# Kernel optimization log

Measured on AMD Instinct MI355X. Metric: run time of the kernel, lower is better.

## Reference

```python
import jax, jax.numpy as jnp
import numpy as np
from jax import lax

B = 1024      # batch
L = 529       # token sequence length (becomes conv channels after permute)
E = 100       # embedding size (becomes conv steps after permute)
V = 15245     # vocab size
F = 16        # conv filters
U = 100       # LSTM units
ALPHA = 0.2   # leaky_relu negative slope (keras.ops.leaky_relu default)


def setup_inputs() -> dict:
    key = jax.random.key(0)
    ks = jax.random.split(key, 8)
    tokens = jax.random.randint(ks[0], (B, L), 0, V)
    # Embedding: keras 'uniform' initializer (-0.05, 0.05)
    emb = jax.random.uniform(ks[1], (V, E), minval=-0.05, maxval=0.05, dtype=jnp.float32)
    # Conv1D kernel [width, in_ch, out_ch], HeNormal
    conv_w = jax.random.normal(ks[2], (2, L, F), dtype=jnp.float32) * np.sqrt(2.0 / (2 * L))
    conv_b = jnp.zeros((F,), jnp.float32)
    # LSTM kernels: [in, 4U] and [U, 4U], gate order i,f,g,o; unit_forget_bias=1
    k_lstm = jax.random.normal(ks[3], (F, 4 * U), dtype=jnp.float32) * np.sqrt(1.0 / F)
    rk_lstm = jax.random.normal(ks[4], (U, 4 * U), dtype=jnp.float32) * np.sqrt(1.0 / U)
    b_lstm = jnp.concatenate([jnp.zeros((U,)), jnp.ones((U,)), jnp.zeros((2 * U,))]).astype(jnp.float32)
    w1 = jax.random.normal(ks[5], (U, 64), dtype=jnp.float32) * np.sqrt(1.0 / U)
    b1 = jnp.zeros((64,), jnp.float32)
    w2 = jax.random.normal(ks[6], (64, 3), dtype=jnp.float32) * np.sqrt(1.0 / 64)
    b2 = jnp.zeros((3,), jnp.float32)
    return dict(tokens=tokens, emb=emb, conv_w=conv_w, conv_b=conv_b,
                k_lstm=k_lstm, rk_lstm=rk_lstm, b_lstm=b_lstm,
                w1=w1, b1=b1, w2=w2, b2=b2)


def _leaky(v):
    return jnp.where(v >= 0, v, ALPHA * v)


def reference(tokens, emb, conv_w, conv_b, k_lstm, rk_lstm, b_lstm, w1, b1, w2, b2):
    x = emb[tokens]                       # [B, 529, 100]
    x = jnp.transpose(x, (0, 2, 1))       # [B, 100, 529]  (steps=100, channels=529)
    x = lax.conv_general_dilated(x, conv_w, window_strides=(2,), padding='SAME',
                                 dimension_numbers=('NWC', 'WIO', 'NWC'))
    x = jax.nn.relu(x + conv_b)           # [B, 50, 16]
    b, lo, c = x.shape
    x = x.reshape(b, lo // 2, 2, c).max(axis=2)  # max_pool k=2 s=2 -> [B, 25, 16]

    # LSTM with activation=leaky_relu, recurrent_activation=sigmoid, gates i,f,g,o
    zx = jnp.einsum('btc,cu->btu', x, k_lstm) + b_lstm  # precompute input proj [B, 25, 4U]

    def step(carry, z_t):
        h, cst = carry
        z = z_t + h @ rk_lstm
        i, f, g, o = jnp.split(z, 4, axis=-1)
        i = jax.nn.sigmoid(i)
        f = jax.nn.sigmoid(f)
        o = jax.nn.sigmoid(o)
        cst = f * cst + i * _leaky(g)
        h = o * _leaky(cst)
        return (h, cst), None

    h0 = jnp.zeros((b, U), x.dtype)
    (h, _), _ = lax.scan(step, (h0, h0), jnp.swapaxes(zx, 0, 1))  # scan over 25 steps

    d = jnp.tanh(h @ w1 + b1)             # dropout is identity at inference
    return jax.nn.softmax(d @ w2 + b2, axis=-1)  # [B, 3]
```

## Files before the change

### kernel.cpp

```cpp
#include <hip/hip_runtime.h>
#include <hip/hip_bf16.h>

#define B_  1024
#define LA  529
#define EE  100
#define NF  16
#define NT  50
#define NS  25
#define NU  100
#define NJ  400
#define NKC 34

typedef float        f32x4v __attribute__((ext_vector_type(4)));
typedef short        s16x8  __attribute__((ext_vector_type(8)));
typedef unsigned int u32x4  __attribute__((ext_vector_type(4)));
typedef _Float16     h2v    __attribute__((ext_vector_type(2)));
typedef _Float16     h16x8  __attribute__((ext_vector_type(8)));

__device__ __forceinline__ float leaky(float v) { return v >= 0.f ? v : 0.2f * v; }

__device__ __forceinline__ unsigned int pkh2(float x, float y) {
    auto p = __builtin_amdgcn_cvt_pkrtz(x, y);
    return __builtin_bit_cast(unsigned int, p);
}
__device__ __forceinline__ unsigned short f2h(float x) {
    return __builtin_bit_cast(unsigned short, (_Float16)x);
}

__global__ __launch_bounds__(256) void prep_kernel(
    const float* __restrict__ emb,
    const float* __restrict__ conv_w,
    const float* __restrict__ k_lstm,
    const float* __restrict__ rk,
    const float* __restrict__ b_lstm,
    unsigned int*   __restrict__ emb_h,
    unsigned int*   __restrict__ convw_h,
    unsigned short* __restrict__ wfl)
{
    const int gid = blockIdx.x * 256 + threadIdx.x;
    const int stride = gridDim.x * 256;
    for (int i = gid; i < (15245 * 100) / 2; i += stride) {
        const float2 v = ((const float2*)emb)[i];
        emb_h[i] = pkh2(v.x, v.y);
    }
    for (int i = gid; i < LA * NF; i += stride)
        convw_h[i] = pkh2(conv_w[i], conv_w[LA * NF + i]);
    for (int n = gid; n < 25 * 2048; n += stride) {
        const int tile = n >> 11, c = (n >> 9) & 3, l = (n >> 3) & 63, e = n & 7;
        const int jg = tile * 16 + (l & 15);
        const int k  = c * 32 + ((l >> 4) << 3) + e;
        float x = 0.f;
        if (k < NU)        x = rk[k * NJ + jg];
        else if (k < 116)  x = k_lstm[(k - NU) * NJ + jg];
        else if (k == 116) x = b_lstm[jg];
        wfl[n] = f2h(x);
    }
}

__global__ __launch_bounds__(256, 2) void conv_mfma_kernel(
    const int*          __restrict__ tokens,
    const unsigned int* __restrict__ emb_h,
    const unsigned int* __restrict__ convw_h,
    const float*        __restrict__ conv_b,
    float*              __restrict__ p_out)
{
    __shared__ __align__(16) unsigned int wf[NKC * 64 * 4];
    __shared__ int tok2[2 * LA];

    const int tid  = threadIdx.x;
    const int lane = tid & 63;
    const int wid  = tid >> 6;
    const int bb   = wid >> 1;
    const int tp   = wid & 1;
    const int b    = blockIdx.x * 2 + bb;

    if (tid < 256) {
        const int j = tid & 3, l = (tid >> 2) & 63;
        if (!(((l >> 4) == 0) && (j == 0)))
            wf[(NKC - 1) * 256 + tid] = 0u;
    }
    for (int i = tid; i < LA * NF; i += 256) {
        const int c = i >> 4, f = i & 15;
        wf[(((c >> 4) * 64 + ((c >> 2) & 3) * 16 + f) << 2) + (c & 3)] = convw_h[i];
    }
    for (int i = tid; i < 2 * LA; i += 256)
        tok2[i] = tokens[(size_t)blockIdx.x * 2 * LA + i];
    __syncthreads();

    const int r = lane & 15;
    const int q = lane >> 4;
    const int m0 = tp * 2, m1 = m0 + 1;
    int tr0 = m0 * 16 + r; tr0 = tr0 > 49 ? 49 : tr0;
    int tr1 = m1 * 16 + r; tr1 = tr1 > 49 ? 49 : tr1;
    const int* __restrict__ tk = tok2 + bb * LA;

    f32x4v ac0 = {0.f, 0.f, 0.f, 0.f}, ac1 = {0.f, 0.f, 0.f, 0.f};

#define LOAD_A(s_, A0, A1) do { \
    const int s2 = (s_); \
    _Pragma("unroll") \
    for (int j = 0; j < 4; ++j) { \
        int c = 16 * s2 + 4 * q + j; \
        if (c >= LA) c = 0; \
        const size_t rowb = (size_t)tk[c] * 50; \
        (A0)[j] = emb_h[rowb + tr0]; \
        (A1)[j] = emb_h[rowb + tr1]; \
    } } while (0)

    u32x4 Aa0, Aa1, Ab0, Ab1, An0, An1;
    LOAD_A(0, Aa0, Aa1);
    LOAD_A(1, Ab0, Ab1);
#pragma unroll
    for (int s = 0; s < NKC; ++s) {
        if (s + 2 < NKC) LOAD_A(s + 2, An0, An1);
        const u32x4 Bv = ((const u32x4*)wf)[s * 64 + lane];
        ac0 = __builtin_amdgcn_mfma_f32_16x16x32_f16(
            __builtin_bit_cast(h16x8, Aa0), __builtin_bit_cast(h16x8, Bv), ac0, 0, 0, 0);
        ac1 = __builtin_amdgcn_mfma_f32_16x16x32_f16(
            __builtin_bit_cast(h16x8, Aa1), __builtin_bit_cast(h16x8, Bv), ac1, 0, 0, 0);
        Aa0 = Ab0; Aa1 = Ab1; Ab0 = An0; Ab1 = An1;
    }
#undef LOAD_A

    const float bf = conv_b[r];
    {
        const float y0 = fmaxf(ac0[0] + bf, 0.f), y1 = fmaxf(ac0[1] + bf, 0.f);
        const float y2 = fmaxf(ac0[2] + bf, 0.f), y3 = fmaxf(ac0[3] + bf, 0.f);
        const int s0 = m0 * 8 + 2 * q;
        if (s0 < NS)     p_out[(size_t)b * (NS * NF) + s0 * NF + r]       = fmaxf(y0, y1);
        if (s0 + 1 < NS) p_out[(size_t)b * (NS * NF) + (s0 + 1) * NF + r] = fmaxf(y2, y3);
    }
    {
        const float y0 = fmaxf(ac1[0] + bf, 0.f), y1 = fmaxf(ac1[1] + bf, 0.f);
        const float y2 = fmaxf(ac1[2] + bf, 0.f), y3 = fmaxf(ac1[3] + bf, 0.f);
        const int s0 = m1 * 8 + 2 * q;
        if (s0 < NS)     p_out[(size_t)b * (NS * NF) + s0 * NF + r]       = fmaxf(y0, y1);
        if (s0 + 1 < NS) p_out[(size_t)b * (NS * NF) + (s0 + 1) * NF + r] = fmaxf(y2, y3);
    }
}

__global__ __launch_bounds__(896) void lstm_mfma_kernel(
    const float* __restrict__ p_in,
    const unsigned short* __restrict__ wfl,
    const float* __restrict__ w1,
    const float* __restrict__ b1,
    const float* __restrict__ w2,
    const float* __restrict__ b2,
    float*       __restrict__ out)
{
    __shared__ __align__(16) unsigned short a_lds[2][4][64][8];
    __shared__ __align__(16) float z_lds[NJ][4];
    __shared__ float h_f32[4][NU];
    __shared__ float d_lds[4 * 64];

    const int tid  = threadIdx.x;
    const int lane = tid & 63;
    const int wid  = tid >> 6;
    const int b0   = blockIdx.x * 4;

    for (int i = tid; i < 2 * 4 * 64 * 8; i += 896) ((unsigned short*)a_lds)[i] = 0;

    const int t0 = (wid * 2     < 25) ? wid * 2     : 0;
    const int t1 = (wid * 2 + 1 < 25) ? wid * 2 + 1 : 0;
    h16x8 bfr[2][4];
#pragma unroll
    for (int c = 0; c < 4; ++c) {
        bfr[0][c] = __builtin_bit_cast(h16x8,
            ((const s16x8*)wfl)[(t0 * 4 + c) * 64 + lane]);
        bfr[1][c] = __builtin_bit_cast(h16x8,
            ((const s16x8*)wfl)[(t1 * 4 + c) * 64 + lane]);
    }
    __syncthreads();

    if (tid < 64) {
        const int pb = tid >> 4, pf = tid & 15;
        const float pv = p_in[(size_t)(b0 + pb) * (NS * NF) + pf];
        const int k = 100 + pf;
        a_lds[0][k >> 5][(((k >> 3) & 3) << 4) + pb][k & 7] = f2h(pv);
    }
    if (tid < 4) {
        a_lds[0][3][32 + tid][4] = 0x3C00;
        a_lds[1][3][32 + tid][4] = 0x3C00;
    }
    float cst = 0.f;
    const int gb = tid & 3, gu = tid >> 2;
    __syncthreads();

#pragma unroll 1
    for (int t = 0; t < NS; ++t) {
        const int cur = t & 1, nxt = cur ^ 1;
        float pv = 0.f;
        if (tid >= 832 && t + 1 < NS) {
            const int idx = tid - 832, pb = idx >> 4, pf = idx & 15;
            pv = p_in[(size_t)(b0 + pb) * (NS * NF) + (t + 1) * NF + pf];
        }
        if (wid < 13) {
            h16x8 ah[4];
#pragma unroll
            for (int c = 0; c < 4; ++c)
                ah[c] = __builtin_bit_cast(h16x8, ((const s16x8*)a_lds[cur][c])[lane]);
#pragma unroll
            for (int i = 0; i < 2; ++i) {
                const int ntg = wid * 2 + i;
                if (ntg < 25) {
                    f32x4v z0 = {0.f, 0.f, 0.f, 0.f}, z1 = {0.f, 0.f, 0.f, 0.f};
                    z0 = __builtin_amdgcn_mfma_f32_16x16x32_f16(ah[0], bfr[i][0], z0, 0, 0, 0);
                    z1 = __builtin_amdgcn_mfma_f32_16x16x32_f16(ah[1], bfr[i][1], z1, 0, 0, 0);
                    z0 = __builtin_amdgcn_mfma_f32_16x16x32_f16(ah[2], bfr[i][2], z0, 0, 0, 0);
                    z1 = __builtin_amdgcn_mfma_f32_16x16x32_f16(ah[3], bfr[i][3], z1, 0, 0, 0);
                    const f32x4v acc = z0 + z1;
                    if (lane < 16) {
                        *((f32x4v*)z_lds[ntg * 16 + lane]) = acc;
                    }
                }
            }
        }
        __syncthreads();
        if (tid < 4 * NU) {
            const float zi = z_lds[gu][gb];
            const float zf = z_lds[gu + 100][gb];
            const float zg = z_lds[gu + 200][gb];
            const float zo = z_lds[gu + 300][gb];
            const float ig  = 1.f / (1.f + __expf(-zi));
            const float fg_ = 1.f / (1.f + __expf(-zf));
            const float og  = 1.f / (1.f + __expf(-zo));
            cst = fg_ * cst + ig * leaky(zg);
            const float h = og * leaky(cst);
            h_f32[gb][gu] = h;
            const int c = gu >> 5, ls = (((gu >> 3) & 3) << 4) + gb, e = gu & 7;
            a_lds[nxt][c][ls][e] = f2h(h);
        }
        if (tid >= 832 && t + 1 < NS) {
            const int idx = tid - 832, pb = idx >> 4, pf = idx & 15;
            const int k = 100 + pf;
            a_lds[nxt][k >> 5][(((k >> 3) & 3) << 4) + pb][k & 7] = f2h(pv);
        }
        __syncthreads();
    }

    if (tid < 256) {
        const int hb = tid >> 6, m = tid & 63;
        float a = b1[m];
#pragma unroll 4
        for (int u = 0; u < NU; ++u) a += h_f32[hb][u] * w1[u * 64 + m];
        d_lds[hb * 64 + m] = tanhf(a);
    }
    __syncthreads();

    if (tid < 4) {
        float l0 = b2[0], l1 = b2[1], l2 = b2[2];
        for (int m = 0; m < 64; ++m) {
            const float d = d_lds[tid * 64 + m];
            l0 += d * w2[m * 3 + 0];
            l1 += d * w2[m * 3 + 1];
            l2 += d * w2[m * 3 + 2];
        }
        const float mx = fmaxf(l0, fmaxf(l1, l2));
        const float e0 = __expf(l0 - mx), e1 = __expf(l1 - mx), e2 = __expf(l2 - mx);
        const float inv = 1.f / (e0 + e1 + e2);
        out[(b0 + tid) * 3 + 0] = e0 * inv;
        out[(b0 + tid) * 3 + 1] = e1 * inv;
        out[(b0 + tid) * 3 + 2] = e2 * inv;
    }
}

extern "C" void kernel_launch(void* const* d_in, const int* in_sizes, int n_in,
                              void* d_out, int out_size, void* d_ws, size_t ws_size,
                              hipStream_t stream) {
    const int*   tokens = (const int*)  d_in[0];
    const float* emb    = (const float*)d_in[1];
    const float* conv_w = (const float*)d_in[2];
    const float* conv_b = (const float*)d_in[3];
    const float* k_lstm = (const float*)d_in[4];
    const float* rk     = (const float*)d_in[5];
    const float* b_lstm = (const float*)d_in[6];
    const float* w1     = (const float*)d_in[7];
    const float* b1     = (const float*)d_in[8];
    const float* w2     = (const float*)d_in[9];
    const float* b2     = (const float*)d_in[10];
    float* out = (float*)d_out;

    char* ws = (char*)d_ws;
    float*          p_ws    = (float*)ws;
    unsigned int*   emb_h   = (unsigned int*)(ws + 1638400);
    unsigned int*   convw_h = (unsigned int*)(ws + 4687408);
    unsigned short* wfl     = (unsigned short*)(ws + 4721280);

    prep_kernel<<<1024, 256, 0, stream>>>(emb, conv_w, k_lstm, rk, b_lstm,
                                          emb_h, convw_h, wfl);
    conv_mfma_kernel<<<B_ / 2, 256, 0, stream>>>(tokens, emb_h, convw_h, conv_b, p_ws);
    lstm_mfma_kernel<<<B_ / 4, 896, 0, stream>>>(p_ws, wfl, w1, b1, w2, b2, out);
}
```

Before: 53.31 us.

## Fuse LSTM gate math into MFMA waves by regrouping weight tiles per unit

Weight tiles are re-laid out so each of 7 waves computes the i,f,g,o gate columns for the same 16 units. The gate nonlinearity and cell update can then run directly on the MFMA accumulators in registers. This removes the z_lds round trip and one of the two barriers per timestep, and shrinks the block from 896 to 512 threads, with one wave reserved for prefetching the next input projection. In exchange each wave does 16 MFMAs per step instead of 8, only 16 of 64 lanes write results, and the last tile pads units 100 to 111 with zeros.

```diff
diff --git a/kernel.cpp b/kernel.cpp
--- a/kernel.cpp
+++ b/kernel.cpp
@@ -45,14 +45,18 @@
     }
     for (int i = gid; i < LA * NF; i += stride)
         convw_h[i] = pkh2(conv_w[i], conv_w[LA * NF + i]);
-    for (int n = gid; n < 25 * 2048; n += stride) {
-        const int tile = n >> 11, c = (n >> 9) & 3, l = (n >> 3) & 63, e = n & 7;
-        const int jg = tile * 16 + (l & 15);
+    for (int n = gid; n < 28 * 2048; n += stride) {
+        const int tt = n >> 11, c = (n >> 9) & 3, l = (n >> 3) & 63, e = n & 7;
+        const int g = tt / 7, ut = tt - g * 7;
+        const int jl = ut * 16 + (l & 15);
         const int k  = c * 32 + ((l >> 4) << 3) + e;
         float x = 0.f;
-        if (k < NU)        x = rk[k * NJ + jg];
-        else if (k < 116)  x = k_lstm[(k - NU) * NJ + jg];
-        else if (k == 116) x = b_lstm[jg];
+        if (jl < NU) {
+            const int jg = g * NU + jl;
+            if (k < NU)        x = rk[k * NJ + jg];
+            else if (k < 116)  x = k_lstm[(k - NU) * NJ + jg];
+            else if (k == 116) x = b_lstm[jg];
+        }
         wfl[n] = f2h(x);
     }
 }
@@ -139,7 +143,7 @@
     }
 }
 
-__global__ __launch_bounds__(896) void lstm_mfma_kernel(
+__global__ __launch_bounds__(512) void lstm_mfma_kernel(
     const float* __restrict__ p_in,
     const unsigned short* __restrict__ wfl,
     const float* __restrict__ w1,
@@ -149,7 +153,6 @@
     float*       __restrict__ out)
 {
     __shared__ __align__(16) unsigned short a_lds[2][4][64][8];
-    __shared__ __align__(16) float z_lds[NJ][4];
     __shared__ float h_f32[4][NU];
     __shared__ float d_lds[4 * 64];
 
@@ -157,19 +160,20 @@
     const int lane = tid & 63;
     const int wid  = tid >> 6;
     const int b0   = blockIdx.x * 4;
-
-    for (int i = tid; i < 2 * 4 * 64 * 8; i += 896) ((unsigned short*)a_lds)[i] = 0;
-
-    const int t0 = (wid * 2     < 25) ? wid * 2     : 0;
-    const int t1 = (wid * 2 + 1 < 25) ? wid * 2 + 1 : 0;
-    h16x8 bfr[2][4];
-#pragma unroll
-    for (int c = 0; c < 4; ++c) {
-        bfr[0][c] = __builtin_bit_cast(h16x8,
-            ((const s16x8*)wfl)[(t0 * 4 + c) * 64 + lane]);
-        bfr[1][c] = __builtin_bit_cast(h16x8,
-            ((const s16x8*)wfl)[(t1 * 4 + c) * 64 + lane]);
-    }
+    const int col  = lane & 15;
+
+    for (int i = tid; i < 2 * 4 * 64 * 8; i += 512) ((unsigned short*)a_lds)[i] = 0;
+
+    const int widc = wid < 7 ? wid : 0;
+    const int jl   = (wid < 7 ? wid : 6) * 16 + col;
+    const bool uvalid = (wid < 7) && (jl < NU) && ((lane >> 4) == 0);
+    h16x8 bfr[4][4];
+#pragma unroll
+    for (int g = 0; g < 4; ++g)
+#pragma unroll
+        for (int c = 0; c < 4; ++c)
+            bfr[g][c] = __builtin_bit_cast(h16x8,
+                ((const s16x8*)wfl)[((g * 7 + widc) * 4 + c) * 64 + lane]);
     __syncthreads();
 
     if (tid < 64) {
@@ -182,58 +186,52 @@
         a_lds[0][3][32 + tid][4] = 0x3C00;
         a_lds[1][3][32 + tid][4] = 0x3C00;
     }
-    float cst = 0.f;
-    const int gb = tid & 3, gu = tid >> 2;
+    float cst[4] = {0.f, 0.f, 0.f, 0.f};
+    const int c_  = jl >> 5;
+    const int lsb = ((jl >> 3) & 3) << 4;
+    const int e_  = jl & 7;
     __syncthreads();
 
 #pragma unroll 1
     for (int t = 0; t < NS; ++t) {
         const int cur = t & 1, nxt = cur ^ 1;
-        float pv = 0.f;
-        if (tid >= 832 && t + 1 < NS) {
-            const int idx = tid - 832, pb = idx >> 4, pf = idx & 15;
-            pv = p_in[(size_t)(b0 + pb) * (NS * NF) + (t + 1) * NF + pf];
-        }
-        if (wid < 13) {
+        if (wid == 7) {
+            if (t + 1 < NS) {
+                const int pb = lane >> 4, pf = lane & 15;
+                const float pv =
+                    p_in[(size_t)(b0 + pb) * (NS * NF) + (t + 1) * NF + pf];
+                const int k = 100 + pf;
+                a_lds[nxt][k >> 5][(((k >> 3) & 3) << 4) + pb][k & 7] = f2h(pv);
+            }
+        } else {
             h16x8 ah[4];
 #pragma unroll
             for (int c = 0; c < 4; ++c)
                 ah[c] = __builtin_bit_cast(h16x8, ((const s16x8*)a_lds[cur][c])[lane]);
-#pragma unroll
-            for (int i = 0; i < 2; ++i) {
-                const int ntg = wid * 2 + i;
-                if (ntg < 25) {
-                    f32x4v z0 = {0.f, 0.f, 0.f, 0.f}, z1 = {0.f, 0.f, 0.f, 0.f};
-                    z0 = __builtin_amdgcn_mfma_f32_16x16x32_f16(ah[0], bfr[i][0], z0, 0, 0, 0);
-                    z1 = __builtin_amdgcn_mfma_f32_16x16x32_f16(ah[1], bfr[i][1], z1, 0, 0, 0);
-                    z0 = __builtin_amdgcn_mfma_f32_16x16x32_f16(ah[2], bfr[i][2], z0, 0, 0, 0);
-                    z1 = __builtin_amdgcn_mfma_f32_16x16x32_f16(ah[3], bfr[i][3], z1, 0, 0, 0);
-                    const f32x4v acc = z0 + z1;
-                    if (lane < 16) {
-                        *((f32x4v*)z_lds[ntg * 16 + lane]) = acc;
-                    }
+            f32x4v acc[4];
+#pragma unroll
+            for (int g = 0; g < 4; ++g) {
+                f32x4v z0 = {0.f, 0.f, 0.f, 0.f}, z1 = {0.f, 0.f, 0.f, 0.f};
+                z0 = __builtin_amdgcn_mfma_f32_16x16x32_f16(ah[0], bfr[g][0], z0, 0, 0, 0);
+                z1 = __builtin_amdgcn_mfma_f32_16x16x32_f16(ah[1], bfr[g][1], z1, 0, 0, 0);
+                z0 = __builtin_amdgcn_mfma_f32_16x16x32_f16(ah[2], bfr[g][2], z0, 0, 0, 0);
+                z1 = __builtin_amdgcn_mfma_f32_16x16x32_f16(ah[3], bfr[g][3], z1, 0, 0, 0);
+                acc[g] = z0 + z1;
+            }
+#pragma unroll
+            for (int q = 0; q < 4; ++q) {
+                const float zi = acc[0][q], zf = acc[1][q];
+                const float zg = acc[2][q], zo = acc[3][q];
+                const float ig  = 1.f / (1.f + __expf(-zi));
+                const float fg_ = 1.f / (1.f + __expf(-zf));
+                const float og  = 1.f / (1.f + __expf(-zo));
+                cst[q] = fg_ * cst[q] + ig * leaky(zg);
+                const float h = og * leaky(cst[q]);
+                if (uvalid) {
+                    a_lds[nxt][c_][lsb + q][e_] = f2h(h);
+                    if (t == NS - 1) h_f32[q][jl] = h;
                 }
             }
-        }
-        __syncthreads();
-        if (tid < 4 * NU) {
-            const float zi = z_lds[gu][gb];
-            const float zf = z_lds[gu + 100][gb];
-            const float zg = z_lds[gu + 200][gb];
-            const float zo = z_lds[gu + 300][gb];
-            const float ig  = 1.f / (1.f + __expf(-zi));
-            const float fg_ = 1.f / (1.f + __expf(-zf));
-            const float og  = 1.f / (1.f + __expf(-zo));
-            cst = fg_ * cst + ig * leaky(zg);
-            const float h = og * leaky(cst);
-            h_f32[gb][gu] = h;
-            const int c = gu >> 5, ls = (((gu >> 3) & 3) << 4) + gb, e = gu & 7;
-            a_lds[nxt][c][ls][e] = f2h(h);
-        }
-        if (tid >= 832 && t + 1 < NS) {
-            const int idx = tid - 832, pb = idx >> 4, pf = idx & 15;
-            const int k = 100 + pf;
-            a_lds[nxt][k >> 5][(((k >> 3) & 3) << 4) + pb][k & 7] = f2h(pv);
         }
         __syncthreads();
     }
@@ -289,5 +287,5 @@
     prep_kernel<<<1024, 256, 0, stream>>>(emb, conv_w, k_lstm, rk, b_lstm,
                                           emb_h, convw_h, wfl);
     conv_mfma_kernel<<<B_ / 2, 256, 0, stream>>>(tokens, emb_h, convw_h, conv_b, p_ws);
-    lstm_mfma_kernel<<<B_ / 4, 896, 0, stream>>>(p_ws, wfl, w1, b1, w2, b2, out);
-}
+    lstm_mfma_kernel<<<B_ / 4, 512, 0, stream>>>(p_ws, wfl, w1, b1, w2, b2, out);
+}
```

Result: slower. 65.72 us (+23.3%).

## Map one batch row per conv block with one M-tile per wave

Applied to the files above, without the earlier changes.

The conv kernel now launches one block per batch element instead of two. Each of the four waves owns a single 16-row M tile rather than two, and MFMA accumulation alternates between two accumulators to break the dependency chain. Launch bounds are raised to allow four blocks per CU. The aim is more parallelism, fewer registers per thread and better latency hiding. The cost is that every block redoes the LDS weight staging, which now happens twice as often overall.

```diff
diff --git a/kernel.cpp b/kernel.cpp
--- a/kernel.cpp
+++ b/kernel.cpp
@@ -57,7 +57,7 @@
     }
 }
 
-__global__ __launch_bounds__(256, 2) void conv_mfma_kernel(
+__global__ __launch_bounds__(256, 4) void conv_mfma_kernel(
     const int*          __restrict__ tokens,
     const unsigned int* __restrict__ emb_h,
     const unsigned int* __restrict__ convw_h,
@@ -65,16 +65,14 @@
     float*              __restrict__ p_out)
 {
     __shared__ __align__(16) unsigned int wf[NKC * 64 * 4];
-    __shared__ int tok2[2 * LA];
+    __shared__ int tokl[LA];
 
     const int tid  = threadIdx.x;
     const int lane = tid & 63;
-    const int wid  = tid >> 6;
-    const int bb   = wid >> 1;
-    const int tp   = wid & 1;
-    const int b    = blockIdx.x * 2 + bb;
-
-    if (tid < 256) {
+    const int m    = __builtin_amdgcn_readfirstlane(tid >> 6);
+    const int b    = blockIdx.x;
+
+    {
         const int j = tid & 3, l = (tid >> 2) & 63;
         if (!(((l >> 4) == 0) && (j == 0)))
             wf[(NKC - 1) * 256 + tid] = 0u;
@@ -83,60 +81,49 @@
         const int c = i >> 4, f = i & 15;
         wf[(((c >> 4) * 64 + ((c >> 2) & 3) * 16 + f) << 2) + (c & 3)] = convw_h[i];
     }
-    for (int i = tid; i < 2 * LA; i += 256)
-        tok2[i] = tokens[(size_t)blockIdx.x * 2 * LA + i];
+    for (int i = tid; i < LA; i += 256)
+        tokl[i] = tokens[(size_t)b * LA + i];
     __syncthreads();
 
     const int r = lane & 15;
     const int q = lane >> 4;
-    const int m0 = tp * 2, m1 = m0 + 1;
-    int tr0 = m0 * 16 + r; tr0 = tr0 > 49 ? 49 : tr0;
-    int tr1 = m1 * 16 + r; tr1 = tr1 > 49 ? 49 : tr1;
-    const int* __restrict__ tk = tok2 + bb * LA;
-
-    f32x4v ac0 = {0.f, 0.f, 0.f, 0.f}, ac1 = {0.f, 0.f, 0.f, 0.f};
-
-#define LOAD_A(s_, A0, A1) do { \
+    int tr = m * 16 + r; tr = tr > 49 ? 49 : tr;
+
+    f32x4v z0 = {0.f, 0.f, 0.f, 0.f}, z1 = {0.f, 0.f, 0.f, 0.f};
+
+#define LOAD_A(s_, A0) do { \
     const int s2 = (s_); \
     _Pragma("unroll") \
     for (int j = 0; j < 4; ++j) { \
         int c = 16 * s2 + 4 * q + j; \
         if (c >= LA) c = 0; \
-        const size_t rowb = (size_t)tk[c] * 50; \
-        (A0)[j] = emb_h[rowb + tr0]; \
-        (A1)[j] = emb_h[rowb + tr1]; \
+        (A0)[j] = emb_h[(size_t)tokl[c] * 50 + tr]; \
     } } while (0)
 
-    u32x4 Aa0, Aa1, Ab0, Ab1, An0, An1;
-    LOAD_A(0, Aa0, Aa1);
-    LOAD_A(1, Ab0, Ab1);
+    u32x4 Aa, Ab, An;
+    LOAD_A(0, Aa);
+    LOAD_A(1, Ab);
 #pragma unroll
     for (int s = 0; s < NKC; ++s) {
-        if (s + 2 < NKC) LOAD_A(s + 2, An0, An1);
+        if (s + 2 < NKC) LOAD_A(s + 2, An);
         const u32x4 Bv = ((const u32x4*)wf)[s * 64 + lane];
-        ac0 = __builtin_amdgcn_mfma_f32_16x16x32_f16(
-            __builtin_bit_cast(h16x8, Aa0), __builtin_bit_cast(h16x8, Bv), ac0, 0, 0, 0);
-        ac1 = __builtin_amdgcn_mfma_f32_16x16x32_f16(
-            __builtin_bit_cast(h16x8, Aa1), __builtin_bit_cast(h16x8, Bv), ac1, 0, 0, 0);
-        Aa0 = Ab0; Aa1 = Ab1; Ab0 = An0; Ab1 = An1;
+        if (s & 1)
+            z1 = __builtin_amdgcn_mfma_f32_16x16x32_f16(
+                __builtin_bit_cast(h16x8, Aa), __builtin_bit_cast(h16x8, Bv), z1, 0, 0, 0);
+        else
+            z0 = __builtin_amdgcn_mfma_f32_16x16x32_f16(
+                __builtin_bit_cast(h16x8, Aa), __builtin_bit_cast(h16x8, Bv), z0, 0, 0, 0);
+        Aa = Ab; Ab = An;
     }
 #undef LOAD_A
+    const f32x4v ac = z0 + z1;
 
     const float bf = conv_b[r];
-    {
-        const float y0 = fmaxf(ac0[0] + bf, 0.f), y1 = fmaxf(ac0[1] + bf, 0.f);
-        const float y2 = fmaxf(ac0[2] + bf, 0.f), y3 = fmaxf(ac0[3] + bf, 0.f);
-        const int s0 = m0 * 8 + 2 * q;
-        if (s0 < NS)     p_out[(size_t)b * (NS * NF) + s0 * NF + r]       = fmaxf(y0, y1);
-        if (s0 + 1 < NS) p_out[(size_t)b * (NS * NF) + (s0 + 1) * NF + r] = fmaxf(y2, y3);
-    }
-    {
-        const float y0 = fmaxf(ac1[0] + bf, 0.f), y1 = fmaxf(ac1[1] + bf, 0.f);
-        const float y2 = fmaxf(ac1[2] + bf, 0.f), y3 = fmaxf(ac1[3] + bf, 0.f);
-        const int s0 = m1 * 8 + 2 * q;
-        if (s0 < NS)     p_out[(size_t)b * (NS * NF) + s0 * NF + r]       = fmaxf(y0, y1);
-        if (s0 + 1 < NS) p_out[(size_t)b * (NS * NF) + (s0 + 1) * NF + r] = fmaxf(y2, y3);
-    }
+    const float y0 = fmaxf(ac[0] + bf, 0.f), y1 = fmaxf(ac[1] + bf, 0.f);
+    const float y2 = fmaxf(ac[2] + bf, 0.f), y3 = fmaxf(ac[3] + bf, 0.f);
+    const int s0 = m * 8 + 2 * q;
+    if (s0 < NS)     p_out[(size_t)b * (NS * NF) + s0 * NF + r]       = fmaxf(y0, y1);
+    if (s0 + 1 < NS) p_out[(size_t)b * (NS * NF) + (s0 + 1) * NF + r] = fmaxf(y2, y3);
 }
 
 __global__ __launch_bounds__(896) void lstm_mfma_kernel(
@@ -288,6 +275,6 @@
 
     prep_kernel<<<1024, 256, 0, stream>>>(emb, conv_w, k_lstm, rk, b_lstm,
                                           emb_h, convw_h, wfl);
-    conv_mfma_kernel<<<B_ / 2, 256, 0, stream>>>(tokens, emb_h, convw_h, conv_b, p_ws);
+    conv_mfma_kernel<<<B_, 256, 0, stream>>>(tokens, emb_h, convw_h, conv_b, p_ws);
     lstm_mfma_kernel<<<B_ / 4, 896, 0, stream>>>(p_ws, wfl, w1, b1, w2, b2, out);
 }
```

Result: no change. 53.92 us (+1.1%).
